# Kernel tuning notes

Measured on AMD Instinct MI355X. Metric: run time of the kernel, lower is better.

Reference implementation:

```python
import jax, jax.numpy as jnp
import numpy as np
import itertools

N = 65536          # points
R = 1.0 / 16.0     # radius (forward uses 1/16)
K = 64             # max_num_neighbors in forward call
G = 16             # grid cells per axis (cell size == R)


def _radius_knn_edges(pts):
    """Grid-hashed radius search; per point keep nearest K within R (self-loop included),
    pad with self index so every point has exactly K edges (max-aggregation neutral)."""
    cells = np.minimum((pts / R).astype(np.int64), G - 1)
    cid = (cells[:, 0] * G + cells[:, 1]) * G + cells[:, 2]
    order = np.argsort(cid, kind='stable')
    sorted_cid = cid[order]
    counts = np.bincount(cid, minlength=G ** 3)
    starts = np.concatenate([[0], np.cumsum(counts)[:-1]])
    M = int(counts.max())
    cand = -np.ones((G ** 3, M), dtype=np.int64)
    slot = np.arange(N) - starts[sorted_cid]
    cand[sorted_cid, slot] = order
    offs = np.array(list(itertools.product([-1, 0, 1], repeat=3)))
    nbr = np.empty((N, K), dtype=np.int64)
    chunk = 4096
    for s in range(0, N, chunk):
        e = min(s + chunk, N)
        c = cells[s:e]
        nc = c[:, None, :] + offs[None]                      # [B,27,3]
        valid_c = np.all((nc >= 0) & (nc < G), axis=-1)      # [B,27]
        ncid = (nc[..., 0] * G + nc[..., 1]) * G + nc[..., 2]
        ncid = np.where(valid_c, ncid, 0)
        cd = cand[ncid]                                      # [B,27,M]
        cd = np.where(np.broadcast_to(valid_c[..., None], cd.shape), cd, -1)
        cd = cd.reshape(e - s, -1)                           # [B,27M]
        p = pts[np.maximum(cd, 0)]
        d = np.linalg.norm(p - pts[s:e, None, :], axis=-1)
        d = np.where((cd >= 0) & (d <= R), d, np.inf)
        sel = np.argsort(d, axis=1)[:, :K]
        row = np.arange(e - s)[:, None]
        picked = cd[row, sel]
        ok = np.isfinite(d[row, sel])
        nbr[s:e] = np.where(ok, picked, np.arange(s, e)[:, None])
    out_index = np.repeat(np.arange(N, dtype=np.int64), K)
    in_index = nbr.reshape(-1)
    return out_index, in_index


def setup_inputs() -> dict:
    key = jax.random.key(0)
    ks = jax.random.split(key, 16)
    pos = jax.random.uniform(ks[0], (N, 3), dtype=jnp.float32)
    rgb = jax.random.uniform(ks[1], (N, 3), dtype=jnp.float32)
    batch = jnp.zeros((N,), dtype=jnp.int64)
    oi, ii = _radius_knn_edges(np.asarray(pos, dtype=np.float64))
    out_index = jnp.asarray(oi)
    in_index = jnp.asarray(ii)

    def lin_w(k, fi, fo):
        return jax.random.normal(k, (fi, fo), dtype=jnp.float32) / np.sqrt(fi).astype(np.float32)

    def lin_b(k, fo):
        return 0.01 * jax.random.normal(k, (fo,), dtype=jnp.float32)

    return {
        'pos': pos, 'rgb': rgb, 'batch': batch,
        'out_index': out_index, 'in_index': in_index,
        'w1a': lin_w(ks[2], 6, 8),   'b1a': lin_b(ks[3], 8),
        'w1b': lin_w(ks[4], 8, 8),   'b1b': lin_b(ks[5], 8),
        'w2a': lin_w(ks[6], 11, 16), 'b2a': lin_b(ks[7], 16),
        'w2b': lin_w(ks[8], 16, 16), 'b2b': lin_b(ks[9], 16),
        'w3a': lin_w(ks[10], 19, 32), 'b3a': lin_b(ks[11], 32),
        'w3b': lin_w(ks[12], 32, 32), 'b3b': lin_b(ks[13], 32),
    }


def _point_conv(x, pos, out_index, in_index, wa, ba, wb, bb):
    # gather neighbor features + relative position, local MLP, max-scatter, output linear
    dpos = pos[in_index] - pos[out_index]                      # [E,3]
    msg = jnp.concatenate([x[in_index], dpos], axis=-1)        # [E,c_in+3]
    h = jax.nn.celu(msg @ wa + ba)                             # [E,c_mid]
    agg = jax.ops.segment_max(h, out_index, num_segments=pos.shape[0],
                              indices_are_sorted=True)         # [N,c_mid]
    return agg @ wb + bb                                       # [N,c_out]


def reference(pos, rgb, batch, out_index, in_index,
              w1a, b1a, w1b, b1b, w2a, b2a, w2b, b2b, w3a, b3a, w3b, b3b):
    out = jax.nn.celu(_point_conv(pos, pos, out_index, in_index, w1a, b1a, w1b, b1b))
    out = jax.nn.celu(_point_conv(out, pos, out_index, in_index, w2a, b2a, w2b, b2b))
    out = jax.nn.celu(_point_conv(out, pos, out_index, in_index, w3a, b3a, w3b, b3b))
    return (pos, out, batch)
```

## Files before the change

### kernel.cpp

```cpp
#include <hip/hip_runtime.h>
#include <hip/hip_fp16.h>
#include <math.h>


#define NPTS 65536
#define KNBR 64
#define TILE 32

__device__ __forceinline__ float celu1(float x) {
    return x > 0.0f ? x : (__expf(x) - 1.0f);
}

__device__ __forceinline__ unsigned pkmax(unsigned a, unsigned b) {
    unsigned d;
    asm("v_pk_max_f16 %0, %1, %2" : "=v"(d) : "v"(a), "v"(b));
    return d;
}

__device__ __forceinline__ unsigned pack2(float a, float b) {
    __half2 h = __floats2half2_rn(a, b);
    return *(unsigned*)&h;
}

__global__ __launch_bounds__(256) void k_prep(
    const float* __restrict__ pos,
    const float* __restrict__ w1a,
    const float* __restrict__ b1a,
    __half* __restrict__ q1,
    float* __restrict__ dout,
    int out_size)
{
    int t = blockIdx.x * 256 + threadIdx.x;
    if (t >= NPTS) return;
    float p0 = pos[3 * t + 0];
    float p1 = pos[3 * t + 1];
    float p2 = pos[3 * t + 2];
    dout[3 * t + 0] = p0;
    dout[3 * t + 1] = p1;
    dout[3 * t + 2] = p2;
    float q[8];
#pragma unroll
    for (int c = 0; c < 8; ++c) {
        float a = b1a[c];
        a = fmaf(p0, w1a[0 * 8 + c] + w1a[3 * 8 + c], a);
        a = fmaf(p1, w1a[1 * 8 + c] + w1a[4 * 8 + c], a);
        a = fmaf(p2, w1a[2 * 8 + c] + w1a[5 * 8 + c], a);
        q[c] = a;
    }
    uint4 pk;
    pk.x = pack2(q[0], q[1]);
    pk.y = pack2(q[2], q[3]);
    pk.z = pack2(q[4], q[5]);
    pk.w = pack2(q[6], q[7]);
    *(uint4*)(q1 + 8 * t) = pk;
    for (int j = 35 * NPTS + t; j < out_size; j += NPTS)
        dout[j] = 0.0f;
}

template <int FH, int FOUT, int FHN, bool WRITEX>
__global__ __launch_bounds__(256, 8) void k_layer(
    const __half* __restrict__ q,
    const int* __restrict__ idx,
    const float* __restrict__ pos,
    const float* __restrict__ wap,
    const float* __restrict__ wb,
    const float* __restrict__ bb,
    const float* __restrict__ wan,
    const float* __restrict__ ban,
    float* __restrict__ xout,
    __half* __restrict__ qnext)
{
    constexpr int SL  = FH / 8;
    constexpr int LPP = SL * 8;
    constexpr int PPW = 64 / LPP;
    constexpr int NIT = TILE / (4 * PPW);

    __shared__ uint4 m_lds[TILE * SL];

    int w  = threadIdx.x >> 6;
    int l  = threadIdx.x & 63;
    int pl = l / LPP;
    int u  = l % LPP;
    int c  = u % SL;
    int g  = u / SL;
    int pbase = blockIdx.x * TILE;

#pragma unroll
    for (int it = 0; it < NIT; ++it) {
        int lp = it * (4 * PPW) + w * PPW + pl;
        int p  = pbase + lp;
        const uint4* ip = (const uint4*)(idx + p * KNBR + g * 8);
        uint4 i0 = ip[0];
        uint4 i1 = ip[1];
        uint4 v[8];
        v[0] = *(const uint4*)(q + (int)i0.x * FH + c * 8);
        v[1] = *(const uint4*)(q + (int)i0.y * FH + c * 8);
        v[2] = *(const uint4*)(q + (int)i0.z * FH + c * 8);
        v[3] = *(const uint4*)(q + (int)i0.w * FH + c * 8);
        v[4] = *(const uint4*)(q + (int)i1.x * FH + c * 8);
        v[5] = *(const uint4*)(q + (int)i1.y * FH + c * 8);
        v[6] = *(const uint4*)(q + (int)i1.z * FH + c * 8);
        v[7] = *(const uint4*)(q + (int)i1.w * FH + c * 8);

        unsigned ax = 0xFC00FC00u, ay = 0xFC00FC00u, az = 0xFC00FC00u, aw = 0xFC00FC00u;
#pragma unroll
        for (int k = 0; k < 8; ++k) {
            ax = pkmax(ax, v[k].x);
            ay = pkmax(ay, v[k].y);
            az = pkmax(az, v[k].z);
            aw = pkmax(aw, v[k].w);
        }
#pragma unroll
        for (int st = SL; st < LPP; st <<= 1) {
            ax = pkmax(ax, (unsigned)__shfl_xor((int)ax, st, 64));
            ay = pkmax(ay, (unsigned)__shfl_xor((int)ay, st, 64));
            az = pkmax(az, (unsigned)__shfl_xor((int)az, st, 64));
            aw = pkmax(aw, (unsigned)__shfl_xor((int)aw, st, 64));
        }
        if (g == 0) {
            uint4 r; r.x = ax; r.y = ay; r.z = az; r.w = aw;
            m_lds[lp * SL + c] = r;
        }
    }
    __syncthreads();

    if constexpr (WRITEX) {
        if (threadIdx.x < TILE * 4) {
            int pt  = threadIdx.x >> 2;
            int qtr = threadIdx.x & 3;
            int p   = pbase + pt;
            float p0 = pos[3 * p + 0];
            float p1 = pos[3 * p + 1];
            float p2 = pos[3 * p + 2];

            float h[FH];
#pragma unroll
            for (int s = 0; s < SL; ++s) {
                uint4 vv = m_lds[pt * SL + s];
                unsigned w4[4] = {vv.x, vv.y, vv.z, vv.w};
#pragma unroll
                for (int k = 0; k < 4; ++k) {
                    float2 f = __half22float2(*(__half2*)&w4[k]);
                    h[s * 8 + k * 2 + 0] = f.x;
                    h[s * 8 + k * 2 + 1] = f.y;
                }
            }
#pragma unroll
            for (int ch = 0; ch < FH; ++ch) {
                float gg = p0 * wap[ch] + p1 * wap[FH + ch] + p2 * wap[2 * FH + ch];
                h[ch] = celu1(h[ch] - gg);
            }
            float x[8];
#pragma unroll
            for (int j = 0; j < 8; ++j) {
                int c2 = qtr * 8 + j;
                float a = bb[c2];
#pragma unroll
                for (int ch = 0; ch < FH; ++ch)
                    a = fmaf(h[ch], wb[ch * FOUT + c2], a);
                x[j] = celu1(a);
            }
            float4* xo = (float4*)(xout + (long long)p * FOUT + qtr * 8);
            xo[0] = make_float4(x[0], x[1], x[2], x[3]);
            xo[1] = make_float4(x[4], x[5], x[6], x[7]);
        }
    } else if (threadIdx.x < TILE) {
        int lt = threadIdx.x;
        int p  = pbase + lt;
        float p0 = pos[3 * p + 0];
        float p1 = pos[3 * p + 1];
        float p2 = pos[3 * p + 2];

        float h[FH];
#pragma unroll
        for (int s = 0; s < SL; ++s) {
            uint4 vv = m_lds[lt * SL + s];
            unsigned w4[4] = {vv.x, vv.y, vv.z, vv.w};
#pragma unroll
            for (int k = 0; k < 4; ++k) {
                float2 f = __half22float2(*(__half2*)&w4[k]);
                h[s * 8 + k * 2 + 0] = f.x;
                h[s * 8 + k * 2 + 1] = f.y;
            }
        }
#pragma unroll
        for (int ch = 0; ch < FH; ++ch) {
            float gg = p0 * wap[ch] + p1 * wap[FH + ch] + p2 * wap[2 * FH + ch];
            h[ch] = celu1(h[ch] - gg);
        }
        float x[FOUT];
#pragma unroll
        for (int c2 = 0; c2 < FOUT; ++c2) {
            float a = bb[c2];
#pragma unroll
            for (int ch = 0; ch < FH; ++ch)
                a = fmaf(h[ch], wb[ch * FOUT + c2], a);
            x[c2] = celu1(a);
        }
        if constexpr (FHN > 0) {
            uint4* qo = (uint4*)(qnext + p * FHN);
#pragma unroll
            for (int s = 0; s < FHN / 8; ++s) {
                float qn[8];
#pragma unroll
                for (int k = 0; k < 8; ++k) {
                    int cn = s * 8 + k;
                    float a = ban[cn];
#pragma unroll
                    for (int c2 = 0; c2 < FOUT; ++c2)
                        a = fmaf(x[c2], wan[c2 * FHN + cn], a);
                    a = fmaf(p0, wan[(FOUT + 0) * FHN + cn], a);
                    a = fmaf(p1, wan[(FOUT + 1) * FHN + cn], a);
                    a = fmaf(p2, wan[(FOUT + 2) * FHN + cn], a);
                    qn[k] = a;
                }
                uint4 pk;
                pk.x = pack2(qn[0], qn[1]);
                pk.y = pack2(qn[2], qn[3]);
                pk.z = pack2(qn[4], qn[5]);
                pk.w = pack2(qn[6], qn[7]);
                qo[s] = pk;
            }
        }
    }
}

extern "C" void kernel_launch(void* const* d_in, const int* in_sizes, int n_in,
                              void* d_out, int out_size, void* d_ws, size_t ws_size,
                              hipStream_t stream) {
    const float* pos = (const float*)d_in[0];
    const int* idx = (const int*)d_in[4];
    const float* w1a = (const float*)d_in[5];
    const float* b1a = (const float*)d_in[6];
    const float* w1b = (const float*)d_in[7];
    const float* b1b = (const float*)d_in[8];
    const float* w2a = (const float*)d_in[9];
    const float* b2a = (const float*)d_in[10];
    const float* w2b = (const float*)d_in[11];
    const float* b2b = (const float*)d_in[12];
    const float* w3a = (const float*)d_in[13];
    const float* b3a = (const float*)d_in[14];
    const float* w3b = (const float*)d_in[15];
    const float* b3b = (const float*)d_in[16];
    float* out = (float*)d_out;

    char* ws = (char*)d_ws;
    __half* A = (__half*)ws;
    __half* B = (__half*)(ws + (4u << 20));

    k_prep<<<NPTS / 256, 256, 0, stream>>>(pos, w1a, b1a, A, out, out_size);
    k_layer<8, 8, 16, false><<<NPTS / TILE, 256, 0, stream>>>(
        A, idx, pos, w1a + 3 * 8, w1b, b1b, w2a, b2a, nullptr, B);
    k_layer<16, 16, 32, false><<<NPTS / TILE, 256, 0, stream>>>(
        B, idx, pos, w2a + 8 * 16, w2b, b2b, w3a, b3a, nullptr, A);
    k_layer<32, 32, 0, true><<<NPTS / TILE, 256, 0, stream>>>(
        A, idx, pos, w3a + 16 * 32, w3b, b3b, nullptr, nullptr, out + 3 * NPTS, nullptr);
}
```

Before: 178.0 us.

## Reorder points by spatial grid cell to improve neighbor gather locality

Adds a counting-sort pass (histogram, scan, atomic scatter) that permutes points into grid-cell order, and rewrites the neighbor index table into the permuted numbering so the per-layer gathers hit nearby memory. The layer kernels read sorted positions and features, and the final layer scatters its outputs back to the original point order. Block indices are also swizzled so that blocks running at the same time cover spread-out cells. This adds several extra kernels plus a full 16 MB index transform per call. Because the scatter uses atomics, the order of points within a cell is nondeterministic, though the results do not depend on it.

```diff
diff --git a/kernel.cpp b/kernel.cpp
--- a/kernel.cpp
+++ b/kernel.cpp
@@ -6,6 +6,7 @@
 #define NPTS 65536
 #define KNBR 64
 #define TILE 32
+#define NCELL 4096
 
 __device__ __forceinline__ float celu1(float x) {
     return x > 0.0f ? x : (__expf(x) - 1.0f);
@@ -22,39 +23,101 @@
     return *(unsigned*)&h;
 }
 
-__global__ __launch_bounds__(256) void k_prep(
-    const float* __restrict__ pos,
-    const float* __restrict__ w1a,
-    const float* __restrict__ b1a,
-    __half* __restrict__ q1,
-    float* __restrict__ dout,
-    int out_size)
+
+__global__ __launch_bounds__(256) void k_cell(
+    const float* __restrict__ pos, float* __restrict__ dout, int out_size,
+    int* __restrict__ cid, int* __restrict__ hist)
+{
+    int t = blockIdx.x * 256 + threadIdx.x;
+    if (t < NPTS) {
+        float p0 = pos[3 * t + 0];
+        float p1 = pos[3 * t + 1];
+        float p2 = pos[3 * t + 2];
+        dout[3 * t + 0] = p0;
+        dout[3 * t + 1] = p1;
+        dout[3 * t + 2] = p2;
+        int cx = min((int)(p0 * 16.0f), 15);
+        int cy = min((int)(p1 * 16.0f), 15);
+        int cz = min((int)(p2 * 16.0f), 15);
+        int c = (cx * 16 + cy) * 16 + cz;
+        cid[t] = c;
+        atomicAdd(&hist[c], 1);
+        for (int j = 35 * NPTS + t; j < out_size; j += NPTS)
+            dout[j] = 0.0f;
+    }
+}
+
+__global__ __launch_bounds__(64) void k_scan(
+    const int* __restrict__ hist, int* __restrict__ cellptr)
+{
+    int l = threadIdx.x;
+    int v[64];
+    int s = 0;
+#pragma unroll
+    for (int i = 0; i < 64; ++i) { v[i] = s; s += hist[l * 64 + i]; }
+    int run = s;
+#pragma unroll
+    for (int st = 1; st < 64; st <<= 1) {
+        int o = __shfl_up(run, st, 64);
+        if (l >= st) run += o;
+    }
+    int off = run - s;
+#pragma unroll
+    for (int i = 0; i < 64; ++i)
+        cellptr[l * 64 + i] = off + v[i];
+}
+
+__global__ __launch_bounds__(256) void k_scatter(
+    const float* __restrict__ pos, const int* __restrict__ cid,
+    int* __restrict__ cellptr, unsigned short* __restrict__ perm,
+    int* __restrict__ order, float* __restrict__ pos_s,
+    const float* __restrict__ w1a, const float* __restrict__ b1a,
+    __half* __restrict__ q1s)
 {
     int t = blockIdx.x * 256 + threadIdx.x;
     if (t >= NPTS) return;
+    int c = cid[t];
+    int nid = atomicAdd(&cellptr[c], 1);
+    perm[t] = (unsigned short)nid;
+    order[nid] = t;
     float p0 = pos[3 * t + 0];
     float p1 = pos[3 * t + 1];
     float p2 = pos[3 * t + 2];
-    dout[3 * t + 0] = p0;
-    dout[3 * t + 1] = p1;
-    dout[3 * t + 2] = p2;
+    pos_s[3 * nid + 0] = p0;
+    pos_s[3 * nid + 1] = p1;
+    pos_s[3 * nid + 2] = p2;
     float q[8];
 #pragma unroll
-    for (int c = 0; c < 8; ++c) {
-        float a = b1a[c];
-        a = fmaf(p0, w1a[0 * 8 + c] + w1a[3 * 8 + c], a);
-        a = fmaf(p1, w1a[1 * 8 + c] + w1a[4 * 8 + c], a);
-        a = fmaf(p2, w1a[2 * 8 + c] + w1a[5 * 8 + c], a);
-        q[c] = a;
+    for (int ch = 0; ch < 8; ++ch) {
+        float a = b1a[ch];
+        a = fmaf(p0, w1a[0 * 8 + ch] + w1a[3 * 8 + ch], a);
+        a = fmaf(p1, w1a[1 * 8 + ch] + w1a[4 * 8 + ch], a);
+        a = fmaf(p2, w1a[2 * 8 + ch] + w1a[5 * 8 + ch], a);
+        q[ch] = a;
     }
     uint4 pk;
     pk.x = pack2(q[0], q[1]);
     pk.y = pack2(q[2], q[3]);
     pk.z = pack2(q[4], q[5]);
     pk.w = pack2(q[6], q[7]);
-    *(uint4*)(q1 + 8 * t) = pk;
-    for (int j = 35 * NPTS + t; j < out_size; j += NPTS)
-        dout[j] = 0.0f;
+    *(uint4*)(q1s + 8 * nid) = pk;
+}
+
+__global__ __launch_bounds__(256) void k_trans(
+    const int* __restrict__ idx, const int* __restrict__ order,
+    const unsigned short* __restrict__ perm, int* __restrict__ idxs)
+{
+    int g = blockIdx.x * 256 + threadIdx.x;
+    int row = g >> 4;
+    int j = g & 15;
+    int old = order[row];
+    int4 v = *(const int4*)(idx + old * KNBR + j * 4);
+    int4 o;
+    o.x = perm[v.x];
+    o.y = perm[v.y];
+    o.z = perm[v.z];
+    o.w = perm[v.w];
+    *(int4*)(idxs + row * KNBR + j * 4) = o;
 }
 
 template <int FH, int FOUT, int FHN, bool WRITEX>
@@ -62,6 +125,7 @@
     const __half* __restrict__ q,
     const int* __restrict__ idx,
     const float* __restrict__ pos,
+    const int* __restrict__ order,
     const float* __restrict__ wap,
     const float* __restrict__ wb,
     const float* __restrict__ bb,
@@ -83,7 +147,8 @@
     int u  = l % LPP;
     int c  = u % SL;
     int g  = u / SL;
-    int pbase = blockIdx.x * TILE;
+    int tb = (blockIdx.x & 255) * (NPTS / TILE / 256) + (blockIdx.x >> 8);
+    int pbase = tb * TILE;
 
 #pragma unroll
     for (int it = 0; it < NIT; ++it) {
@@ -160,7 +225,8 @@
                     a = fmaf(h[ch], wb[ch * FOUT + c2], a);
                 x[j] = celu1(a);
             }
-            float4* xo = (float4*)(xout + (long long)p * FOUT + qtr * 8);
+            int oldp = order[p];
+            float4* xo = (float4*)(xout + (long long)oldp * FOUT + qtr * 8);
             xo[0] = make_float4(x[0], x[1], x[2], x[3]);
             xo[1] = make_float4(x[4], x[5], x[6], x[7]);
         }
@@ -245,14 +311,28 @@
     float* out = (float*)d_out;
 
     char* ws = (char*)d_ws;
-    __half* A = (__half*)ws;
-    __half* B = (__half*)(ws + (4u << 20));
-
-    k_prep<<<NPTS / 256, 256, 0, stream>>>(pos, w1a, b1a, A, out, out_size);
+    __half* A      = (__half*)ws;
+    __half* B      = (__half*)(ws + (4u << 20));
+    int*    idxs   = (int*)(ws + (8u << 20));
+    int*    cid    = (int*)(ws + (24u << 20));
+    int*    order  = (int*)(ws + (25u << 20));
+    unsigned short* perm = (unsigned short*)(ws + (26u << 20));
+    int*    hist   = (int*)(ws + (27u << 20));
+    int*    cellptr= (int*)(ws + (27u << 20) + (64u << 10));
+    float*  pos_s  = (float*)(ws + (28u << 20));
+
+    hipMemsetAsync(hist, 0, NCELL * sizeof(int), stream);
+    k_cell<<<NPTS / 256, 256, 0, stream>>>(pos, out, out_size, cid, hist);
+    k_scan<<<1, 64, 0, stream>>>(hist, cellptr);
+    k_scatter<<<NPTS / 256, 256, 0, stream>>>(pos, cid, cellptr, perm, order,
+                                              pos_s, w1a, b1a, A);
+    k_trans<<<NPTS * 16 / 256, 256, 0, stream>>>(idx, order, perm, idxs);
+
     k_layer<8, 8, 16, false><<<NPTS / TILE, 256, 0, stream>>>(
-        A, idx, pos, w1a + 3 * 8, w1b, b1b, w2a, b2a, nullptr, B);
+        A, idxs, pos_s, nullptr, w1a + 3 * 8, w1b, b1b, w2a, b2a, nullptr, B);
     k_layer<16, 16, 32, false><<<NPTS / TILE, 256, 0, stream>>>(
-        B, idx, pos, w2a + 8 * 16, w2b, b2b, w3a, b3a, nullptr, A);
+        B, idxs, pos_s, nullptr, w2a + 8 * 16, w2b, b2b, w3a, b3a, nullptr, A);
     k_layer<32, 32, 0, true><<<NPTS / TILE, 256, 0, stream>>>(
-        A, idx, pos, w3a + 16 * 32, w3b, b3b, nullptr, nullptr, out + 3 * NPTS, nullptr);
-}
+        A, idxs, pos_s, order, w3a + 16 * 32, w3b, b3b, nullptr, nullptr,
+        out + 3 * NPTS, nullptr);
+}
```

After: 177.2 us. Within noise of the previous version (-0.4%).
